# Performance work log

Measured on AMD Instinct MI355X. Metric: run time of the kernel, lower is better.

Reference implementation:

```python
import jax, jax.numpy as jnp
import numpy as np

VARIANCE = (0.1, 0.2)
THRESHOLD = 0.5
NEG_POS = 3


def point_form(boxes):
    # (cx,cy,w,h) -> (xmin,ymin,xmax,ymax)
    return jnp.concatenate([boxes[:, :2] - boxes[:, 2:] / 2,
                            boxes[:, :2] + boxes[:, 2:] / 2], axis=1)


def jaccard(a, b):
    # a: [T,4] xyxy truths, b: [P,4] xyxy priors -> IoU [T,P]
    lt = jnp.maximum(a[:, None, :2], b[None, :, :2])
    rb = jnp.minimum(a[:, None, 2:], b[None, :, 2:])
    wh = jnp.clip(rb - lt, 0.0)
    inter = wh[..., 0] * wh[..., 1]
    area_a = ((a[:, 2] - a[:, 0]) * (a[:, 3] - a[:, 1]))[:, None]
    area_b = ((b[:, 2] - b[:, 0]) * (b[:, 3] - b[:, 1]))[None, :]
    return inter / (area_a + area_b - inter)


def encode(matched, priors):
    g_cxcy = (matched[:, :2] + matched[:, 2:]) / 2 - priors[:, :2]
    g_cxcy = g_cxcy / (VARIANCE[0] * priors[:, 2:])
    g_wh = jnp.log((matched[:, 2:] - matched[:, :2]) / priors[:, 2:]) / VARIANCE[1]
    return jnp.concatenate([g_cxcy, g_wh], axis=1)


def match_one(truths, priors):
    # SSD match for one image; labels are zeroed in BiBoxLoss -> binary conf {0,1}
    overlaps = jaccard(truths, point_form(priors))          # [T,P]
    best_prior_idx = jnp.argmax(overlaps, axis=1)           # [T]
    best_truth_overlap = jnp.max(overlaps, axis=0)          # [P]
    best_truth_idx = jnp.argmax(overlaps, axis=0)           # [P]
    best_truth_overlap = best_truth_overlap.at[best_prior_idx].set(2.0)
    best_truth_idx = best_truth_idx.at[best_prior_idx].set(
        jnp.arange(truths.shape[0]))
    matched = truths[best_truth_idx]                        # [P,4]
    conf = jnp.where(best_truth_overlap < THRESHOLD, 0, 1)  # [P] int
    loc = encode(matched, priors)
    return loc, conf


def bibox_loss(loc_data, conf_data, priors, targets):
    num, num_priors = loc_data.shape[0], loc_data.shape[1]
    truths = targets[..., :4]                               # [B,T,4]
    loc_t, conf_t = jax.vmap(lambda t: match_one(t, priors))(truths)

    pos = conf_t > 0                                        # [B,P]
    # smooth L1 (sum) over positive priors
    ad = jnp.abs(loc_data - loc_t)
    sl1 = jnp.where(ad < 1.0, 0.5 * ad * ad, ad - 0.5)
    loss_l = jnp.sum(sl1 * pos[..., None].astype(loc_data.dtype))

    # per-prior CE (logsumexp - gathered logit) for hard-negative mining
    lse = jax.nn.logsumexp(conf_data, axis=-1)              # [B,P]
    gathered = jnp.take_along_axis(conf_data, conf_t[..., None], axis=-1)[..., 0]
    loss_c_all = lse - gathered                             # [B,P]

    loss_c_mine = jnp.where(pos, 0.0, loss_c_all)
    loss_idx = jnp.argsort(-loss_c_mine, axis=1)
    idx_rank = jnp.argsort(loss_idx, axis=1)                # rank of each prior
    num_pos = jnp.sum(pos.astype(jnp.int32), axis=1, keepdims=True)  # [B,1]
    num_neg = jnp.minimum(NEG_POS * num_pos, num_priors - 1)
    neg = idx_rank < num_neg                                # [B,P]

    sel = pos | neg
    loss_c = jnp.sum(jnp.where(sel, loss_c_all, 0.0))

    N = jnp.sum(num_pos).astype(loc_data.dtype)
    return loss_l / N, loss_c / N


def setup_inputs() -> dict:
    key = jax.random.key(0)
    k1, k2, k3, k4, k5, k6 = jax.random.split(key, 6)
    B, P, T = 32, 65536, 16
    loc_data = jax.random.normal(k1, (B, P, 4), dtype=jnp.float32)
    conf_data = jax.random.normal(k2, (B, P, 2), dtype=jnp.float32)
    # priors: valid center-form boxes
    pc = 0.15 + 0.7 * jax.random.uniform(k3, (P, 2), dtype=jnp.float32)
    pwh = 0.05 + 0.25 * jax.random.uniform(k4, (P, 2), dtype=jnp.float32)
    priors = jnp.concatenate([pc, pwh], axis=1)
    # targets: valid corner-form boxes + dummy label column (zeroed by the loss)
    tc = 0.2 + 0.6 * jax.random.uniform(k5, (B, T, 2), dtype=jnp.float32)
    twh = 0.05 + 0.25 * jax.random.uniform(k6, (B, T, 2), dtype=jnp.float32)
    boxes = jnp.concatenate([tc - twh / 2, tc + twh / 2], axis=-1)
    targets = jnp.concatenate(
        [boxes, jnp.ones((B, T, 1), dtype=jnp.float32)], axis=-1)
    return {"loc_data": loc_data, "conf_data": conf_data,
            "priors": priors, "targets": targets}


def reference(loc_data, conf_data, priors, targets):
    return bibox_loss(loc_data, conf_data, priors, targets)
```

## Files before the change

### kernel.cpp

```cpp
#include <hip/hip_runtime.h>

#define NB_ 32
#define NP_ 65536
#define NT_ 16
#define HB 1024
#define HSCALE 128.0f
#define NBX 64

__device__ __forceinline__ float softplus_(float x) {
    return fmaxf(x, 0.0f) + __logf(1.0f + __expf(-fabsf(x)));
}

__device__ __forceinline__ float iou_fast(float tx0, float ty0, float tx1, float ty1, float ta,
                                          float bx0, float by0, float bx1, float by1, float ar) {
    float lx = fmaxf(tx0, bx0), ly = fmaxf(ty0, by0);
    float rx = fminf(tx1, bx1), ry = fminf(ty1, by1);
    float w = fmaxf(rx - lx, 0.0f), h = fmaxf(ry - ly, 0.0f);
    float inter = w * h;
    return __fdividef(inter, ta + ar - inter);
}

#define DPP_STEP(x, t, ctrl, rmask, bmask, OP)                                          \
    t = __builtin_amdgcn_update_dpp(0, (x), (ctrl), (rmask), (bmask), true); OP;

__device__ __forceinline__ unsigned wave_max_u32(unsigned v) {
    int x = (int)v, t;
    DPP_STEP(x, t, 0x111, 0xf, 0xf, x = ((unsigned)t > (unsigned)x) ? t : x)
    DPP_STEP(x, t, 0x112, 0xf, 0xf, x = ((unsigned)t > (unsigned)x) ? t : x)
    DPP_STEP(x, t, 0x114, 0xf, 0xe, x = ((unsigned)t > (unsigned)x) ? t : x)
    DPP_STEP(x, t, 0x118, 0xf, 0xc, x = ((unsigned)t > (unsigned)x) ? t : x)
    DPP_STEP(x, t, 0x142, 0xa, 0xf, x = ((unsigned)t > (unsigned)x) ? t : x)
    DPP_STEP(x, t, 0x143, 0xc, 0xf, x = ((unsigned)t > (unsigned)x) ? t : x)
    return (unsigned)x;
}

__device__ __forceinline__ float wave_sum_f32(float v) {
    int x = __float_as_int(v), t;
    float f;
    DPP_STEP(x, t, 0x111, 0xf, 0xf, f = __int_as_float(x) + __int_as_float(t); x = __float_as_int(f))
    DPP_STEP(x, t, 0x112, 0xf, 0xf, f = __int_as_float(x) + __int_as_float(t); x = __float_as_int(f))
    DPP_STEP(x, t, 0x114, 0xf, 0xe, f = __int_as_float(x) + __int_as_float(t); x = __float_as_int(f))
    DPP_STEP(x, t, 0x118, 0xf, 0xc, f = __int_as_float(x) + __int_as_float(t); x = __float_as_int(f))
    DPP_STEP(x, t, 0x142, 0xa, 0xf, f = __int_as_float(x) + __int_as_float(t); x = __float_as_int(f))
    DPP_STEP(x, t, 0x143, 0xc, 0xf, f = __int_as_float(x) + __int_as_float(t); x = __float_as_int(f))
    return __int_as_float(x);
}

__device__ __forceinline__ int wave_sum_i32(int v) {
    int x = v, t;
    DPP_STEP(x, t, 0x111, 0xf, 0xf, x = x + t)
    DPP_STEP(x, t, 0x112, 0xf, 0xf, x = x + t)
    DPP_STEP(x, t, 0x114, 0xf, 0xe, x = x + t)
    DPP_STEP(x, t, 0x118, 0xf, 0xc, x = x + t)
    DPP_STEP(x, t, 0x142, 0xa, 0xf, x = x + t)
    DPP_STEP(x, t, 0x143, 0xc, 0xf, x = x + t)
    return x;
}

__global__ void __launch_bounds__(256) mainK(
    const float* __restrict__ loc, const float* __restrict__ conf,
    const float* __restrict__ priors, const float* __restrict__ targets,
    unsigned short* __restrict__ gcnt, float* __restrict__ gsum,
    unsigned long long* __restrict__ bestPart,
    float* __restrict__ part_ll, float* __restrict__ part_pc, int* __restrict__ part_np)
{
    const int bx = blockIdx.x, b = blockIdx.y, tid = threadIdx.x;

    __shared__ float4 trb[NT_];
    __shared__ float tra[NT_];
    __shared__ int hc[HB];
    __shared__ float hs[HB];
    __shared__ unsigned wkey[4][NT_], wp[4][NT_];
    __shared__ float sh_ll[4], sh_pc[4];
    __shared__ int sh_np[4];

    for (int i = tid; i < HB; i += 256) { hc[i] = 0; hs[i] = 0.0f; }
    if (tid < NT_) {
        const float* tp = targets + ((size_t)b * NT_ + tid) * 5;
        float x0 = tp[0], y0 = tp[1], x1 = tp[2], y1 = tp[3];
        trb[tid] = make_float4(x0, y0, x1, y1);
        tra[tid] = (x1 - x0) * (y1 - y0);
    }
    __syncthreads();

    const int pbase = bx * 1024 + tid;
    float pbx0[4], pby0[4], pbx1[4], pby1[4], par[4];
    float2 cxy[4];
#pragma unroll
    for (int i = 0; i < 4; i++) {
        float4 pr = ((const float4*)priors)[pbase + 256 * i];
        cxy[i] = ((const float2*)conf)[(size_t)b * NP_ + pbase + 256 * i];
        float hw = pr.z * 0.5f, hh = pr.w * 0.5f;
        pbx0[i] = pr.x - hw; pby0[i] = pr.y - hh;
        pbx1[i] = pr.x + hw; pby1[i] = pr.y + hh;
        par[i] = (pbx1[i] - pbx0[i]) * (pby1[i] - pby0[i]);
    }

    unsigned pkey[4] = {0u, 0u, 0u, 0u};
    unsigned tkey[NT_];
#pragma unroll
    for (int t = 0; t < NT_; t++) tkey[t] = 0u;

#pragma unroll
    for (int t = 0; t < NT_; t++) {
        float4 tb = trb[t];
        float ta = tra[t];
#pragma unroll
        for (int i = 0; i < 4; i++) {
            float iou = iou_fast(tb.x, tb.y, tb.z, tb.w, ta,
                                 pbx0[i], pby0[i], pbx1[i], pby1[i], par[i]);
            unsigned base = (__float_as_uint(iou) & 0xFFFFFFFCu) << 2;
            unsigned kt = base | (unsigned)(15 - t);
            unsigned kp = base | (unsigned)(15 - i);
            pkey[i] = (kt > pkey[i]) ? kt : pkey[i];
            tkey[t] = (kp > tkey[t]) ? kp : tkey[t];
        }
    }

    float ll_acc = 0.0f, pc_acc = 0.0f;
    int np_acc = 0;
#pragma unroll
    for (int i = 0; i < 4; i++) {
        int p = pbase + 256 * i;
        size_t bp = (size_t)b * NP_ + p;
        bool pos = (pkey[i] >= 0xFC000000u);
        float dd = cxy[i].y - cxy[i].x;
        float v = pos ? 0.0f : softplus_(dd);
        int bin = min(HB - 1, (int)(v * HSCALE));
        atomicAdd(&hc[bin], 1);
        atomicAdd(&hs[bin], v);
        if (pos) {
            np_acc++;
            pc_acc += softplus_(-dd);
            int t = 15 - (int)(pkey[i] & 15u);
            float4 tb = trb[t];
            float4 prv = ((const float4*)priors)[p];
            float gcx = ((tb.x + tb.z) * 0.5f - prv.x) / (0.1f * prv.z);
            float gcy = ((tb.y + tb.w) * 0.5f - prv.y) / (0.1f * prv.w);
            float gw = __logf((tb.z - tb.x) / prv.z) * 5.0f;
            float gh = __logf((tb.w - tb.y) / prv.w) * 5.0f;
            float4 ld = ((const float4*)loc)[bp];
            float d0 = fabsf(ld.x - gcx), d1 = fabsf(ld.y - gcy);
            float d2 = fabsf(ld.z - gw),  d3 = fabsf(ld.w - gh);
            ll_acc += (d0 < 1.0f) ? 0.5f * d0 * d0 : d0 - 0.5f;
            ll_acc += (d1 < 1.0f) ? 0.5f * d1 * d1 : d1 - 0.5f;
            ll_acc += (d2 < 1.0f) ? 0.5f * d2 * d2 : d2 - 0.5f;
            ll_acc += (d3 < 1.0f) ? 0.5f * d3 * d3 : d3 - 0.5f;
        }
    }

    const int wave = tid >> 6, lane = tid & 63;
#pragma unroll
    for (int t = 0; t < NT_; t++) {
        unsigned k = tkey[t];
        unsigned m = (unsigned)__builtin_amdgcn_readlane((int)wave_max_u32(k), 63);
        unsigned long long ball = __ballot(k == m);
        if (lane == 0) {
            int l = __ffsll((long long)ball) - 1;
            int ci = 15 - (int)(m & 15u);
            int p = bx * 1024 + ci * 256 + wave * 64 + l;
            wkey[wave][t] = m;
            wp[wave][t] = (unsigned)p;
        }
    }
    {
        float llw = wave_sum_f32(ll_acc);
        float pcw = wave_sum_f32(pc_acc);
        int npw = wave_sum_i32(np_acc);
        if (lane == 63) { sh_ll[wave] = llw; sh_pc[wave] = pcw; sh_np[wave] = npw; }
    }
    __syncthreads();

    if (tid < NT_) {
        unsigned bk = wkey[0][tid], bpv = wp[0][tid];
        for (int w = 1; w < 4; w++) {
            unsigned k2 = wkey[w][tid], p2 = wp[w][tid];
            if (k2 > bk || (k2 == bk && p2 < bpv)) { bk = k2; bpv = p2; }
        }
        unsigned long long pk = (((unsigned long long)bk) << 32) | (unsigned)(~bpv);
        bestPart[((size_t)b * NT_ + tid) * NBX + bx] = pk;
    }
    if (tid == 0) {
        part_ll[b * NBX + bx] = sh_ll[0] + sh_ll[1] + sh_ll[2] + sh_ll[3];
        part_pc[b * NBX + bx] = sh_pc[0] + sh_pc[1] + sh_pc[2] + sh_pc[3];
        part_np[b * NBX + bx] = sh_np[0] + sh_np[1] + sh_np[2] + sh_np[3];
    }
    unsigned short* gc = gcnt + ((size_t)(b * NBX + bx)) * HB;
    float* gs = gsum + ((size_t)(b * NBX + bx)) * HB;
    for (int i = tid; i < HB; i += 256) { gc[i] = (unsigned short)hc[i]; gs[i] = hs[i]; }
}

__global__ void __launch_bounds__(1024) finishK(
    const float* __restrict__ loc, const float* __restrict__ conf,
    const float* __restrict__ priors, const float* __restrict__ targets,
    const unsigned short* __restrict__ gcnt, const float* __restrict__ gsum,
    const unsigned long long* __restrict__ bestPart,
    const float* __restrict__ part_ll, const float* __restrict__ part_pc,
    const int* __restrict__ part_np,
    float* __restrict__ final_l, float* __restrict__ final_c, int* __restrict__ final_n)
{
    const int b = blockIdx.x, tid = threadIdx.x;
    __shared__ int hc[HB];
    __shared__ float hs[HB];
    __shared__ float4 trb[NT_];
    __shared__ float tra[NT_];
    __shared__ unsigned ps[NT_];
    __shared__ float s_dll, s_dpc, s_sll, s_spc;
    __shared__ int s_dnp, s_sn;
    __shared__ unsigned ccnt[16];
    __shared__ float csm[16];

    if (tid == 0) { s_dll = 0.0f; s_dpc = 0.0f; s_dnp = 0; }
    if (tid < NT_) {
        const float* tp = targets + ((size_t)b * NT_ + tid) * 5;
        float x0 = tp[0], y0 = tp[1], x1 = tp[2], y1 = tp[3];
        trb[tid] = make_float4(x0, y0, x1, y1);
        tra[tid] = (x1 - x0) * (y1 - y0);
    }

    {
        const size_t base = (size_t)(b * NBX) * HB + tid;
        int cA = 0, cB = 0; float sA = 0.0f, sB = 0.0f;
#pragma unroll 8
        for (int j = 0; j < 32; j++) {
            size_t oA = base + (size_t)j * HB;
            size_t oB = base + (size_t)(32 + j) * HB;
            cA += (int)gcnt[oA]; sA += gsum[oA];
            cB += (int)gcnt[oB]; sB += gsum[oB];
        }
        hc[tid] = cA + cB;
        hs[tid] = sA + sB;
    }

    {
        const int tr_i = tid >> 6, lane = tid & 63;
        unsigned long long v = bestPart[((size_t)b * NT_ + tr_i) * NBX + lane];
        for (int off = 32; off > 0; off >>= 1) {
            unsigned long long u = __shfl_down(v, off, 64);
            v = (u > v) ? u : v;
        }
        if (lane == 0) ps[tr_i] = ~((unsigned)(v & 0xffffffffULL));
    }
    if (tid < 64) {
        float lv = part_ll[b * NBX + tid];
        float pv = part_pc[b * NBX + tid];
        int nv = part_np[b * NBX + tid];
        lv = wave_sum_f32(lv); pv = wave_sum_f32(pv); nv = wave_sum_i32(nv);
        if (tid == 63) { s_sll = lv; s_spc = pv; s_sn = nv; }
    }
    __syncthreads();

    if (tid < NT_) {
        unsigned p = ps[tid];
        bool active = true;
        for (int u = tid + 1; u < NT_; u++)
            if (ps[u] == p) { active = false; break; }
        if (active) {
            float4 prv = ((const float4*)priors)[p];
            float hw = prv.z * 0.5f, hh = prv.w * 0.5f;
            float qx0 = prv.x - hw, qy0 = prv.y - hh;
            float qx1 = prv.x + hw, qy1 = prv.y + hh;
            float areab = (qx1 - qx0) * (qy1 - qy0);
            unsigned pk = 0u;
            for (int tt = 0; tt < NT_; tt++) {
                float4 tb = trb[tt];
                float iou = iou_fast(tb.x, tb.y, tb.z, tb.w, tra[tt],
                                     qx0, qy0, qx1, qy1, areab);
                unsigned cand = ((__float_as_uint(iou) & 0xFFFFFFFCu) << 2)
                              | (unsigned)(15 - tt);
                pk = (cand > pk) ? cand : pk;
            }
            bool pos0 = (pk >= 0xFC000000u);
            int t0 = 15 - (int)(pk & 15u);
            size_t bp = (size_t)b * NP_ + p;
            float2 cxyf = ((const float2*)conf)[bp];
            float dd = cxyf.y - cxyf.x;
            float4 ld = ((const float4*)loc)[bp];

            auto sl1_of = [&](int tt) -> float {
                float4 tb = trb[tt];
                float gcx = ((tb.x + tb.z) * 0.5f - prv.x) / (0.1f * prv.z);
                float gcy = ((tb.y + tb.w) * 0.5f - prv.y) / (0.1f * prv.w);
                float gw = __logf((tb.z - tb.x) / prv.z) * 5.0f;
                float gh = __logf((tb.w - tb.y) / prv.w) * 5.0f;
                float d0 = fabsf(ld.x - gcx), d1 = fabsf(ld.y - gcy);
                float d2 = fabsf(ld.z - gw),  d3 = fabsf(ld.w - gh);
                float s = (d0 < 1.0f) ? 0.5f * d0 * d0 : d0 - 0.5f;
                s += (d1 < 1.0f) ? 0.5f * d1 * d1 : d1 - 0.5f;
                s += (d2 < 1.0f) ? 0.5f * d2 * d2 : d2 - 0.5f;
                s += (d3 < 1.0f) ? 0.5f * d3 * d3 : d3 - 0.5f;
                return s;
            };
            float dll = sl1_of(tid) - (pos0 ? sl1_of(t0) : 0.0f);
            atomicAdd(&s_dll, dll);
            if (!pos0) {
                float v = softplus_(dd);
                int bin = min(HB - 1, (int)(v * HSCALE));
                atomicSub(&hc[bin], 1);
                atomicAdd(&hs[bin], -v);
                atomicAdd(&s_dpc, softplus_(-dd));
                atomicAdd(&s_dnp, 1);
            }
        }
    }
    __syncthreads();

    if (tid < 16) {
        unsigned cacc = 0; float sacc = 0.0f;
        for (int j = 0; j < 64; j++) { cacc += (unsigned)hc[tid * 64 + j]; sacc += hs[tid * 64 + j]; }
        ccnt[tid] = cacc; csm[tid] = sacc;
    }
    __syncthreads();

    if (tid == 0) {
        float sll = s_sll + s_dll;
        float spc = s_spc + s_dpc;
        int n = s_sn + s_dnp;
        int K = 3 * n;
        if (K > NP_ - 1) K = NP_ - 1;
        float tk = 0.0f;
        if (K > 0) {
            unsigned need = (unsigned)K, cum = 0;
            float s = 0.0f;
            int cb = 15;
            for (; cb > 0; --cb) {
                if (cum + ccnt[cb] >= need) break;
                cum += ccnt[cb]; s += csm[cb];
            }
            int bin = cb * 64 + 63;
            for (; bin > cb * 64; --bin) {
                if (cum + (unsigned)hc[bin] >= need) break;
                cum += (unsigned)hc[bin]; s += hs[bin];
            }
            unsigned rem = need - cum;
            int cv = hc[bin];
            float avg = (cv > 0) ? __fdividef(hs[bin], (float)cv) : 0.0f;
            tk = s + (float)rem * avg;
        }
        final_l[b] = sll;
        final_c[b] = spc + tk;
        final_n[b] = n;
    }
}

__global__ void __launch_bounds__(64) lastK(
    const float* __restrict__ final_l, const float* __restrict__ final_c,
    const int* __restrict__ final_n, float* __restrict__ out)
{
    const int tid = threadIdx.x;
    float lv = 0.0f, cv = 0.0f;
    int nv = 0;
    if (tid < NB_) { lv = final_l[tid]; cv = final_c[tid]; nv = final_n[tid]; }
    for (int off = 32; off > 0; off >>= 1) {
        lv += __shfl_down(lv, off, 64);
        cv += __shfl_down(cv, off, 64);
        nv += __shfl_down(nv, off, 64);
    }
    if (tid == 0) {
        float fn = (float)nv;
        out[0] = lv / fn;
        out[1] = cv / fn;
    }
}

extern "C" void kernel_launch(void* const* d_in, const int* in_sizes, int n_in,
                              void* d_out, int out_size, void* d_ws, size_t ws_size,
                              hipStream_t stream) {
    const float* loc = (const float*)d_in[0];
    const float* conf = (const float*)d_in[1];
    const float* priors = (const float*)d_in[2];
    const float* targets = (const float*)d_in[3];
    float* out = (float*)d_out;

    char* w = (char*)d_ws;
    unsigned short* gcnt = (unsigned short*)w;
    float* gsum = (float*)(w + (4u << 20));
    char* acc = w + (12u << 20);
    unsigned long long* bestPart = (unsigned long long*)acc;
    float* part_ll = (float*)(acc + 262144);
    float* part_pc = (float*)(acc + 270336);
    int* part_np   = (int*)(acc + 278528);
    float* final_l = (float*)(acc + 286720);
    float* final_c = (float*)(acc + 286848);
    int* final_n   = (int*)(acc + 286976);

    mainK<<<dim3(NBX, NB_), 256, 0, stream>>>(loc, conf, priors, targets,
                                              gcnt, gsum, bestPart,
                                              part_ll, part_pc, part_np);
    finishK<<<NB_, 1024, 0, stream>>>(loc, conf, priors, targets,
                                      gcnt, gsum, bestPart,
                                      part_ll, part_pc, part_np,
                                      final_l, final_c, final_n);
    lastK<<<1, 64, 0, stream>>>(final_l, final_c, final_n, out);
}
```

Measured before the change: 138.2 us.

## Move loss histogram construction from main kernel into per-image finish kernel

```diff
diff --git a/kernel.cpp b/kernel.cpp
--- a/kernel.cpp
+++ b/kernel.cpp
@@ -60,7 +60,7 @@
 __global__ void __launch_bounds__(256) mainK(
     const float* __restrict__ loc, const float* __restrict__ conf,
     const float* __restrict__ priors, const float* __restrict__ targets,
-    unsigned short* __restrict__ gcnt, float* __restrict__ gsum,
+    float* __restrict__ lcm,
     unsigned long long* __restrict__ bestPart,
     float* __restrict__ part_ll, float* __restrict__ part_pc, int* __restrict__ part_np)
 {
@@ -68,13 +68,10 @@
 
     __shared__ float4 trb[NT_];
     __shared__ float tra[NT_];
-    __shared__ int hc[HB];
-    __shared__ float hs[HB];
     __shared__ unsigned wkey[4][NT_], wp[4][NT_];
     __shared__ float sh_ll[4], sh_pc[4];
     __shared__ int sh_np[4];
 
-    for (int i = tid; i < HB; i += 256) { hc[i] = 0; hs[i] = 0.0f; }
     if (tid < NT_) {
         const float* tp = targets + ((size_t)b * NT_ + tid) * 5;
         float x0 = tp[0], y0 = tp[1], x1 = tp[2], y1 = tp[3];
@@ -126,9 +123,7 @@
         bool pos = (pkey[i] >= 0xFC000000u);
         float dd = cxy[i].y - cxy[i].x;
         float v = pos ? 0.0f : softplus_(dd);
-        int bin = min(HB - 1, (int)(v * HSCALE));
-        atomicAdd(&hc[bin], 1);
-        atomicAdd(&hs[bin], v);
+        lcm[bp] = v;
         if (pos) {
             np_acc++;
             pc_acc += softplus_(-dd);
@@ -185,15 +180,12 @@
         part_pc[b * NBX + bx] = sh_pc[0] + sh_pc[1] + sh_pc[2] + sh_pc[3];
         part_np[b * NBX + bx] = sh_np[0] + sh_np[1] + sh_np[2] + sh_np[3];
     }
-    unsigned short* gc = gcnt + ((size_t)(b * NBX + bx)) * HB;
-    float* gs = gsum + ((size_t)(b * NBX + bx)) * HB;
-    for (int i = tid; i < HB; i += 256) { gc[i] = (unsigned short)hc[i]; gs[i] = hs[i]; }
 }
 
 __global__ void __launch_bounds__(1024) finishK(
     const float* __restrict__ loc, const float* __restrict__ conf,
     const float* __restrict__ priors, const float* __restrict__ targets,
-    const unsigned short* __restrict__ gcnt, const float* __restrict__ gsum,
+    const float* __restrict__ lcm,
     const unsigned long long* __restrict__ bestPart,
     const float* __restrict__ part_ll, const float* __restrict__ part_pc,
     const int* __restrict__ part_np,
@@ -217,19 +209,18 @@
         trb[tid] = make_float4(x0, y0, x1, y1);
         tra[tid] = (x1 - x0) * (y1 - y0);
     }
+    hc[tid] = 0; hs[tid] = 0.0f;
+    __syncthreads();
 
     {
-        const size_t base = (size_t)(b * NBX) * HB + tid;
-        int cA = 0, cB = 0; float sA = 0.0f, sB = 0.0f;
+        const float* lp = lcm + (size_t)b * NP_;
 #pragma unroll 8
-        for (int j = 0; j < 32; j++) {
-            size_t oA = base + (size_t)j * HB;
-            size_t oB = base + (size_t)(32 + j) * HB;
-            cA += (int)gcnt[oA]; sA += gsum[oA];
-            cB += (int)gcnt[oB]; sB += gsum[oB];
-        }
-        hc[tid] = cA + cB;
-        hs[tid] = sA + sB;
+        for (int j = 0; j < 64; j++) {
+            float v = lp[tid + 1024 * j];
+            int bin = min(HB - 1, (int)(v * HSCALE));
+            atomicAdd(&hc[bin], 1);
+            atomicAdd(&hs[bin], v);
+        }
     }
 
     {
@@ -373,9 +364,8 @@
     float* out = (float*)d_out;
 
     char* w = (char*)d_ws;
-    unsigned short* gcnt = (unsigned short*)w;
-    float* gsum = (float*)(w + (4u << 20));
-    char* acc = w + (12u << 20);
+    float* lcm = (float*)w;
+    char* acc = w + (8u << 20);
     unsigned long long* bestPart = (unsigned long long*)acc;
     float* part_ll = (float*)(acc + 262144);
     float* part_pc = (float*)(acc + 270336);
@@ -385,10 +375,10 @@
     int* final_n   = (int*)(acc + 286976);
 
     mainK<<<dim3(NBX, NB_), 256, 0, stream>>>(loc, conf, priors, targets,
-                                              gcnt, gsum, bestPart,
+                                              lcm, bestPart,
                                               part_ll, part_pc, part_np);
     finishK<<<NB_, 1024, 0, stream>>>(loc, conf, priors, targets,
-                                      gcnt, gsum, bestPart,
+                                      lcm, bestPart,
                                       part_ll, part_pc, part_np,
                                       final_l, final_c, final_n);
     lastK<<<1, 64, 0, stream>>>(final_l, final_c, final_n, out);
```

Result: slower. 217.0 us (+57.1%).
